# Performance work log

Hardware: AMD Instinct MI355X
Metric: run time of the kernel (lower is better)

The kernel has to match this reference:

```python
import jax, jax.numpy as jnp
import numpy as np

EPS = 1e-06

def rotate_half(x):
    d = x.shape[-1] // 2
    return jnp.concatenate([-x[..., d:], x[..., :d]], axis=-1)

def rmsnorm(x, w):
    rms = jnp.sqrt(jnp.mean(x * x, axis=-1, keepdims=True) + EPS)
    return (x / rms) * w

def setup_inputs() -> dict:
    key = jax.random.key(0)
    ks = jax.random.split(key, 12)
    H, Hq, Hkv, Dh, S, C = 2048, 16, 8, 128, 1, 16384
    sc = 0.02
    return {
        "hidden_states": jax.random.normal(ks[0], (1, 1, S, H), jnp.float32),
        "cos": jax.random.uniform(ks[1], (1, 1, S, Dh), jnp.float32),
        "sin": jax.random.uniform(ks[2], (1, 1, S, Dh), jnp.float32),
        "attention_mask": jnp.zeros((1, 1, S, C + S), jnp.float32),
        "k_cache": jax.random.normal(ks[3], (Hkv, Dh, C), jnp.float32),
        "v_cache": jax.random.normal(ks[4], (Hkv, C, Dh), jnp.float32),
        "Wq": jax.random.normal(ks[5], (Hq, Dh, H), jnp.float32) * sc,
        "Wk": jax.random.normal(ks[6], (Hkv, Dh, H), jnp.float32) * sc,
        "Wv": jax.random.normal(ks[7], (Hkv, Dh, H), jnp.float32) * sc,
        "Wo": jax.random.normal(ks[8], (H, Hq * Dh), jnp.float32) * sc,
        "q_norm_w": jnp.ones((Dh,), jnp.float32),
        "k_norm_w": jnp.ones((Dh,), jnp.float32),
    }

def reference(hidden_states, cos, sin, attention_mask, k_cache, v_cache, Wq, Wk, Wv, Wo, q_norm_w, k_norm_w):
    S = hidden_states.shape[2]
    Hq, Dh = Wq.shape[0], Wq.shape[1]
    Hkv = Wk.shape[0]
    g = Hq // Hkv
    x = hidden_states.reshape(S, -1)                      # [S, H]
    # per-head 1x1 conv == per-head linear; batched as einsum
    q = rmsnorm(jnp.einsum('sh,qdh->qsd', x, Wq), q_norm_w)   # [Hq, S, Dh]
    k = rmsnorm(jnp.einsum('sh,kdh->ksd', x, Wk), k_norm_w)   # [Hkv, S, Dh]
    v = jnp.einsum('sh,kdh->ksd', x, Wv)                      # [Hkv, S, Dh]
    c = cos.reshape(S, Dh)
    s = sin.reshape(S, Dh)
    q = q * c + rotate_half(q) * s
    k_new = k * c + rotate_half(k) * s
    # KV cache concat: k stored transposed [Hkv, Dh, C]
    k_full = jnp.concatenate([k_cache, jnp.swapaxes(k_new, 1, 2)], axis=2)  # [Hkv, Dh, C+S]
    v_full = jnp.concatenate([v_cache, v], axis=1)                          # [Hkv, C+S, Dh]
    kf = jnp.repeat(k_full, g, axis=0)                    # GQA expand -> [Hq, Dh, C+S]
    vf = jnp.repeat(v_full, g, axis=0)                    # [Hq, C+S, Dh]
    scaling = Dh ** -0.5
    scores = jnp.einsum('qsd,qdc->qsc', q, kf) * scaling + attention_mask.reshape(1, S, -1)
    probs = jax.nn.softmax(scores, axis=-1)
    out = jnp.einsum('qsc,qcd->qsd', probs, vf)           # [Hq, S, Dh]
    out = jnp.transpose(out, (1, 0, 2)).reshape(S, Hq * Dh)  # head-major last dim
    attn = out @ Wo.T                                     # o_proj 1x1 conv
    return attn.reshape(1, 1, S, -1), k_new, v
```

## Files before the change

### kernel.cpp

```cpp
#include <hip/hip_runtime.h>
#include <math.h>
#include <stddef.h>

#define HQ   16
#define HKV  8
#define DH   128
#define HID  2048
#define CC   16384
#define NCH  64
#define CHUNK 256


__global__ void k_qkv(const float* __restrict__ x,
                      const float* __restrict__ Wq,
                      const float* __restrict__ Wk,
                      const float* __restrict__ Wv,
                      float* __restrict__ raw){
  int wave = threadIdx.x >> 6, lane = threadIdx.x & 63;
  int e = blockIdx.x * 4 + wave;
  const float* W;
  if (e < 2048)      W = Wq + (size_t)e * HID;
  else if (e < 3072) W = Wk + (size_t)(e - 2048) * HID;
  else               W = Wv + (size_t)(e - 3072) * HID;
  float acc = 0.f;
  #pragma unroll
  for (int j = 0; j < 4; ++j){
    int base = (j * 64 + lane) * 8;
    float4 a0 = *(const float4*)(x + base);
    float4 a1 = *(const float4*)(x + base + 4);
    float4 b0 = *(const float4*)(W + base);
    float4 b1 = *(const float4*)(W + base + 4);
    acc += a0.x*b0.x + a0.y*b0.y + a0.z*b0.z + a0.w*b0.w
         + a1.x*b1.x + a1.y*b1.y + a1.z*b1.z + a1.w*b1.w;
  }
  #pragma unroll
  for (int off = 32; off; off >>= 1) acc += __shfl_down(acc, off, 64);
  if (lane == 0) raw[e] = acc;
}

__global__ void k_normrope(const float* __restrict__ raw,
                           const float* __restrict__ cosb,
                           const float* __restrict__ sinb,
                           const float* __restrict__ qw,
                           const float* __restrict__ kw,
                           float* __restrict__ qf,
                           float* __restrict__ kf,
                           float* __restrict__ out){
  __shared__ float lds[DH];
  __shared__ float wsum[2];
  int b = blockIdx.x, t = threadIdx.x;
  if (b >= 24){
    int h = b - 24;
    out[3072 + h * DH + t] = raw[3072 + h * DH + t];
    return;
  }
  bool isq = (b < 16);
  int h = isq ? b : b - 16;
  float val = isq ? raw[h * DH + t] : raw[2048 + h * DH + t];
  float ss = val * val;
  #pragma unroll
  for (int off = 32; off; off >>= 1) ss += __shfl_down(ss, off, 64);
  if ((t & 63) == 0) wsum[t >> 6] = ss;
  __syncthreads();
  float rms = sqrtf((wsum[0] + wsum[1]) / 128.f + 1e-6f);
  float w = isq ? qw[t] : kw[t];
  float normed = val / rms * w;
  lds[t] = normed;
  __syncthreads();
  float rot = (t < 64) ? -lds[t + 64] : lds[t - 64];
  float res = normed * cosb[t] + rot * sinb[t];
  if (isq) qf[h * DH + t] = res;
  else { kf[h * DH + t] = res; out[2048 + h * DH + t] = res; }
}

__global__ void k_flash(const float* __restrict__ qf,
                        const float* __restrict__ kcache,
                        const float* __restrict__ vcache,
                        const float* __restrict__ mask,
                        float* __restrict__ opart,
                        float2* __restrict__ ml){
  __shared__ float q_s[2][DH];
  __shared__ float sc_part[4][2][CHUNK];
  __shared__ float p_s[2][CHUNK];
  __shared__ float part[2][8][DH];
  __shared__ float red[8];
  int kv = blockIdx.x >> 6, ch = blockIdx.x & 63;
  int c0 = ch << 8;
  int t = threadIdx.x;
  q_s[t >> 7][t & 127] = qf[(kv * 2 + (t >> 7)) * DH + (t & 127)];
  __syncthreads();
  const float scale = 0.08838834764831845f;

  {
    int dg = t >> 6, ln = t & 63;
    const float* kp = kcache + (size_t)kv * DH * CC + (size_t)(dg * 32) * CC + (c0 + ln * 4);
    float a00 = 0.f, a01 = 0.f, a02 = 0.f, a03 = 0.f;
    float a10 = 0.f, a11 = 0.f, a12 = 0.f, a13 = 0.f;
    #pragma unroll 8
    for (int dd = 0; dd < 32; ++dd){
      float4 kk = *(const float4*)(kp + (size_t)dd * CC);
      float q0 = q_s[0][dg * 32 + dd], q1 = q_s[1][dg * 32 + dd];
      a00 += q0 * kk.x; a01 += q0 * kk.y; a02 += q0 * kk.z; a03 += q0 * kk.w;
      a10 += q1 * kk.x; a11 += q1 * kk.y; a12 += q1 * kk.z; a13 += q1 * kk.w;
    }
    *(float4*)&sc_part[dg][0][ln * 4] = make_float4(a00, a01, a02, a03);
    *(float4*)&sc_part[dg][1][ln * 4] = make_float4(a10, a11, a12, a13);
  }
  __syncthreads();

  float s0, s1;
  {
    float mk = mask[c0 + t];
    s0 = (sc_part[0][0][t] + sc_part[1][0][t] + sc_part[2][0][t] + sc_part[3][0][t]) * scale + mk;
    s1 = (sc_part[0][1][t] + sc_part[1][1][t] + sc_part[2][1][t] + sc_part[3][1][t]) * scale + mk;
  }
  int wv = t >> 6, ln = t & 63;
  float lmax0 = s0, lmax1 = s1;
  #pragma unroll
  for (int off = 32; off; off >>= 1){
    lmax0 = fmaxf(lmax0, __shfl_down(lmax0, off, 64));
    lmax1 = fmaxf(lmax1, __shfl_down(lmax1, off, 64));
  }
  if (ln == 0){ red[wv] = lmax0; red[4 + wv] = lmax1; }
  __syncthreads();
  float m0 = fmaxf(fmaxf(red[0], red[1]), fmaxf(red[2], red[3]));
  float m1 = fmaxf(fmaxf(red[4], red[5]), fmaxf(red[6], red[7]));
  float p0 = __expf(s0 - m0);
  float p1 = __expf(s1 - m1);
  p_s[0][t] = p0;
  p_s[1][t] = p1;
  float ls0 = p0, ls1 = p1;
  #pragma unroll
  for (int off = 32; off; off >>= 1){
    ls0 += __shfl_down(ls0, off, 64);
    ls1 += __shfl_down(ls1, off, 64);
  }
  __syncthreads();
  if (ln == 0){ red[wv] = ls0; red[4 + wv] = ls1; }
  __syncthreads();
  if (t == 0){
    float l0 = red[0] + red[1] + red[2] + red[3];
    float l1 = red[4] + red[5] + red[6] + red[7];
    ml[(size_t)(kv * 2)     * NCH + ch] = make_float2(m0, l0);
    ml[(size_t)(kv * 2 + 1) * NCH + ch] = make_float2(m1, l1);
  }

  {
    int s = t >> 5, d4 = (t & 31) * 4;
    const float* vbase = vcache + (size_t)kv * CC * DH + d4;
    float4 a0 = make_float4(0.f, 0.f, 0.f, 0.f);
    float4 a1 = make_float4(0.f, 0.f, 0.f, 0.f);
    #pragma unroll 4
    for (int i = 0; i < 32; ++i){
      int off = i * 8 + s;
      float pp0 = p_s[0][off];
      float pp1 = p_s[1][off];
      float4 v = *(const float4*)(vbase + (size_t)(c0 + off) * DH);
      a0.x += pp0 * v.x; a0.y += pp0 * v.y; a0.z += pp0 * v.z; a0.w += pp0 * v.w;
      a1.x += pp1 * v.x; a1.y += pp1 * v.y; a1.z += pp1 * v.z; a1.w += pp1 * v.w;
    }
    *(float4*)&part[0][s][d4] = a0;
    *(float4*)&part[1][s][d4] = a1;
  }
  __syncthreads();
  {
    int hh = t >> 7, d = t & 127;
    float o = 0.f;
    #pragma unroll
    for (int ss = 0; ss < 8; ++ss) o += part[hh][ss][d];
    int qh = kv * 2 + hh;
    opart[((size_t)qh * NCH + ch) * DH + d] = o;
  }
}

__global__ void k_combine(const float* __restrict__ opart,
                          const float2* __restrict__ ml,
                          const float* __restrict__ qf,
                          const float* __restrict__ kf,
                          const float* __restrict__ vnew,
                          const float* __restrict__ mask,
                          float* __restrict__ attn_in){
  __shared__ float red[2];
  int qh = blockIdx.x, d = threadIdx.x;
  int kv = qh >> 1;
  float M = -1e30f;
  #pragma unroll 8
  for (int ch = 0; ch < NCH; ++ch) M = fmaxf(M, ml[(size_t)qh * NCH + ch].x);
  float o = 0.f, L = 0.f;
  for (int ch = 0; ch < NCH; ++ch){
    float2 m = ml[(size_t)qh * NCH + ch];
    float w = __expf(m.x - M);
    L += m.y * w;
    o += w * opart[((size_t)qh * NCH + ch) * DH + d];
  }
  float prod = qf[qh * DH + d] * kf[kv * DH + d];
  float sum = prod;
  #pragma unroll
  for (int off = 32; off; off >>= 1) sum += __shfl_down(sum, off, 64);
  if ((d & 63) == 0) red[d >> 6] = sum;
  __syncthreads();
  float s_new = (red[0] + red[1]) * 0.08838834764831845f + mask[CC];
  float pn = __expf(s_new - M);
  L += pn;
  o += pn * vnew[kv * DH + d];
  attn_in[qh * DH + d] = o / L;
}

__global__ void k_oproj(const float* __restrict__ attn_in,
                        const float* __restrict__ Wo,
                        float* __restrict__ out){
  int wave = threadIdx.x >> 6, lane = threadIdx.x & 63;
  int e = blockIdx.x * 4 + wave;
  const float* W = Wo + (size_t)e * HID;
  float acc = 0.f;
  #pragma unroll
  for (int j = 0; j < 4; ++j){
    int base = (j * 64 + lane) * 8;
    float4 a0 = *(const float4*)(attn_in + base);
    float4 a1 = *(const float4*)(attn_in + base + 4);
    float4 b0 = *(const float4*)(W + base);
    float4 b1 = *(const float4*)(W + base + 4);
    acc += a0.x*b0.x + a0.y*b0.y + a0.z*b0.z + a0.w*b0.w
         + a1.x*b1.x + a1.y*b1.y + a1.z*b1.z + a1.w*b1.w;
  }
  #pragma unroll
  for (int off = 32; off; off >>= 1) acc += __shfl_down(acc, off, 64);
  if (lane == 0) out[e] = acc;
}

extern "C" void kernel_launch(void* const* d_in, const int* in_sizes, int n_in,
                              void* d_out, int out_size, void* d_ws, size_t ws_size,
                              hipStream_t stream){
  const float* x    = (const float*)d_in[0];
  const float* cosb = (const float*)d_in[1];
  const float* sinb = (const float*)d_in[2];
  const float* mask = (const float*)d_in[3];
  const float* kc   = (const float*)d_in[4];
  const float* vc   = (const float*)d_in[5];
  const float* Wq   = (const float*)d_in[6];
  const float* Wk   = (const float*)d_in[7];
  const float* Wv   = (const float*)d_in[8];
  const float* Wo   = (const float*)d_in[9];
  const float* qw   = (const float*)d_in[10];
  const float* kw   = (const float*)d_in[11];
  float* out = (float*)d_out;
  float* ws = (float*)d_ws;
  float* raw     = ws;
  float* qf      = ws + 4096;
  float* kf      = ws + 6144;
  float* opart   = ws + 8192;
  float2* ML     = (float2*)(ws + 139264);
  float* attn_in = ws + 141312;

  k_qkv     <<<1024, 256, 0, stream>>>(x, Wq, Wk, Wv, raw);
  k_normrope<<<32,   128, 0, stream>>>(raw, cosb, sinb, qw, kw, qf, kf, out);
  k_flash   <<<HKV * NCH, 256, 0, stream>>>(qf, kc, vc, mask, opart, ML);
  k_combine <<<HQ, 128, 0, stream>>>(opart, ML, qf, kf, raw + 3072, mask, attn_in);
  k_oproj   <<<512, 256, 0, stream>>>(attn_in, Wo, out);
}
```

Measured before the change: 216.4 us.

## Halve flash-decode chunk size, parallelize combine, and fuse V-copy into QKV

Splits the KV cache into 128 chunks of 128 positions instead of 64 chunks of 256, which doubles the number of attention blocks (1024) so more of the GPU's compute units are busy streaming K/V. The scoring phase now uses 8 depth groups of 16 per thread, and each head's softmax is reduced within its own half of the block. The combine kernel uses 512 threads, with four groups each merging 32 chunk partials plus a parallel max reduction, to absorb the doubled partial count. The V-output copy is folded into the QKV kernel so the norm/rope launch shrinks to 24 blocks. The cost is twice the partial-output traffic and more combine work.

```diff
diff --git a/kernel.cpp b/kernel.cpp
--- a/kernel.cpp
+++ b/kernel.cpp
@@ -7,15 +7,16 @@
 #define DH   128
 #define HID  2048
 #define CC   16384
-#define NCH  64
-#define CHUNK 256
+#define NCH  128
+#define CHUNK 128
 
 
 __global__ void k_qkv(const float* __restrict__ x,
                       const float* __restrict__ Wq,
                       const float* __restrict__ Wk,
                       const float* __restrict__ Wv,
-                      float* __restrict__ raw){
+                      float* __restrict__ raw,
+                      float* __restrict__ out){
   int wave = threadIdx.x >> 6, lane = threadIdx.x & 63;
   int e = blockIdx.x * 4 + wave;
   const float* W;
@@ -35,7 +36,10 @@
   }
   #pragma unroll
   for (int off = 32; off; off >>= 1) acc += __shfl_down(acc, off, 64);
-  if (lane == 0) raw[e] = acc;
+  if (lane == 0){
+    raw[e] = acc;
+    if (e >= 3072) out[e] = acc;
+  }
 }
 
 __global__ void k_normrope(const float* __restrict__ raw,
@@ -49,11 +53,6 @@
   __shared__ float lds[DH];
   __shared__ float wsum[2];
   int b = blockIdx.x, t = threadIdx.x;
-  if (b >= 24){
-    int h = b - 24;
-    out[3072 + h * DH + t] = raw[3072 + h * DH + t];
-    return;
-  }
   bool isq = (b < 16);
   int h = isq ? b : b - 16;
   float val = isq ? raw[h * DH + t] : raw[2048 + h * DH + t];
@@ -80,26 +79,26 @@
                         float* __restrict__ opart,
                         float2* __restrict__ ml){
   __shared__ float q_s[2][DH];
-  __shared__ float sc_part[4][2][CHUNK];
+  __shared__ float sc_part[8][2][CHUNK];
   __shared__ float p_s[2][CHUNK];
   __shared__ float part[2][8][DH];
   __shared__ float red[8];
-  int kv = blockIdx.x >> 6, ch = blockIdx.x & 63;
-  int c0 = ch << 8;
+  int kv = blockIdx.x >> 7, ch = blockIdx.x & 127;
+  int c0 = ch << 7;
   int t = threadIdx.x;
   q_s[t >> 7][t & 127] = qf[(kv * 2 + (t >> 7)) * DH + (t & 127)];
   __syncthreads();
   const float scale = 0.08838834764831845f;
 
   {
-    int dg = t >> 6, ln = t & 63;
-    const float* kp = kcache + (size_t)kv * DH * CC + (size_t)(dg * 32) * CC + (c0 + ln * 4);
+    int dg = t >> 5, ln = t & 31;
+    const float* kp = kcache + (size_t)kv * DH * CC + (size_t)(dg * 16) * CC + (c0 + ln * 4);
     float a00 = 0.f, a01 = 0.f, a02 = 0.f, a03 = 0.f;
     float a10 = 0.f, a11 = 0.f, a12 = 0.f, a13 = 0.f;
     #pragma unroll 8
-    for (int dd = 0; dd < 32; ++dd){
+    for (int dd = 0; dd < 16; ++dd){
       float4 kk = *(const float4*)(kp + (size_t)dd * CC);
-      float q0 = q_s[0][dg * 32 + dd], q1 = q_s[1][dg * 32 + dd];
+      float q0 = q_s[0][dg * 16 + dd], q1 = q_s[1][dg * 16 + dd];
       a00 += q0 * kk.x; a01 += q0 * kk.y; a02 += q0 * kk.z; a03 += q0 * kk.w;
       a10 += q1 * kk.x; a11 += q1 * kk.y; a12 += q1 * kk.z; a13 += q1 * kk.w;
     }
@@ -108,59 +107,49 @@
   }
   __syncthreads();
 
-  float s0, s1;
-  {
-    float mk = mask[c0 + t];
-    s0 = (sc_part[0][0][t] + sc_part[1][0][t] + sc_part[2][0][t] + sc_part[3][0][t]) * scale + mk;
-    s1 = (sc_part[0][1][t] + sc_part[1][1][t] + sc_part[2][1][t] + sc_part[3][1][t]) * scale + mk;
-  }
-  int wv = t >> 6, ln = t & 63;
-  float lmax0 = s0, lmax1 = s1;
-  #pragma unroll
-  for (int off = 32; off; off >>= 1){
-    lmax0 = fmaxf(lmax0, __shfl_down(lmax0, off, 64));
-    lmax1 = fmaxf(lmax1, __shfl_down(lmax1, off, 64));
-  }
-  if (ln == 0){ red[wv] = lmax0; red[4 + wv] = lmax1; }
-  __syncthreads();
-  float m0 = fmaxf(fmaxf(red[0], red[1]), fmaxf(red[2], red[3]));
-  float m1 = fmaxf(fmaxf(red[4], red[5]), fmaxf(red[6], red[7]));
-  float p0 = __expf(s0 - m0);
-  float p1 = __expf(s1 - m1);
-  p_s[0][t] = p0;
-  p_s[1][t] = p1;
-  float ls0 = p0, ls1 = p1;
-  #pragma unroll
-  for (int off = 32; off; off >>= 1){
-    ls0 += __shfl_down(ls0, off, 64);
-    ls1 += __shfl_down(ls1, off, 64);
-  }
-  __syncthreads();
-  if (ln == 0){ red[wv] = ls0; red[4 + wv] = ls1; }
-  __syncthreads();
-  if (t == 0){
-    float l0 = red[0] + red[1] + red[2] + red[3];
-    float l1 = red[4] + red[5] + red[6] + red[7];
-    ml[(size_t)(kv * 2)     * NCH + ch] = make_float2(m0, l0);
-    ml[(size_t)(kv * 2 + 1) * NCH + ch] = make_float2(m1, l1);
-  }
-
-  {
-    int s = t >> 5, d4 = (t & 31) * 4;
-    const float* vbase = vcache + (size_t)kv * CC * DH + d4;
+  int h = t >> 7, pos = t & 127;
+  float s;
+  {
+    float acc = 0.f;
+    #pragma unroll
+    for (int dg = 0; dg < 8; ++dg) acc += sc_part[dg][h][pos];
+    s = acc * scale + mask[c0 + pos];
+  }
+  int wv = t >> 6;
+  float lm = s;
+  #pragma unroll
+  for (int off = 32; off; off >>= 1) lm = fmaxf(lm, __shfl_down(lm, off, 64));
+  if ((t & 63) == 0) red[wv] = lm;
+  __syncthreads();
+  float m = fmaxf(red[h * 2], red[h * 2 + 1]);
+  float p = __expf(s - m);
+  p_s[h][pos] = p;
+  float lsum = p;
+  #pragma unroll
+  for (int off = 32; off; off >>= 1) lsum += __shfl_down(lsum, off, 64);
+  if ((t & 63) == 0) red[4 + wv] = lsum;
+  __syncthreads();
+  if ((t & 127) == 0){
+    float l = red[4 + h * 2] + red[5 + h * 2];
+    ml[(size_t)(kv * 2 + h) * NCH + ch] = make_float2(m, l);
+  }
+
+  {
+    int sl = t >> 5, d4 = (t & 31) * 4;
+    const float* vbase = vcache + (size_t)kv * CC * DH + (size_t)c0 * DH + d4;
     float4 a0 = make_float4(0.f, 0.f, 0.f, 0.f);
     float4 a1 = make_float4(0.f, 0.f, 0.f, 0.f);
-    #pragma unroll 4
-    for (int i = 0; i < 32; ++i){
-      int off = i * 8 + s;
+    #pragma unroll 8
+    for (int i = 0; i < 16; ++i){
+      int off = i * 8 + sl;
       float pp0 = p_s[0][off];
       float pp1 = p_s[1][off];
-      float4 v = *(const float4*)(vbase + (size_t)(c0 + off) * DH);
+      float4 v = *(const float4*)(vbase + (size_t)off * DH);
       a0.x += pp0 * v.x; a0.y += pp0 * v.y; a0.z += pp0 * v.z; a0.w += pp0 * v.w;
       a1.x += pp1 * v.x; a1.y += pp1 * v.y; a1.z += pp1 * v.z; a1.w += pp1 * v.w;
     }
-    *(float4*)&part[0][s][d4] = a0;
-    *(float4*)&part[1][s][d4] = a1;
+    *(float4*)&part[0][sl][d4] = a0;
+    *(float4*)&part[1][sl][d4] = a1;
   }
   __syncthreads();
   {
@@ -180,30 +169,46 @@
                           const float* __restrict__ vnew,
                           const float* __restrict__ mask,
                           float* __restrict__ attn_in){
-  __shared__ float red[2];
-  int qh = blockIdx.x, d = threadIdx.x;
+  __shared__ float osum[4][DH];
+  __shared__ float Ls[4];
+  __shared__ float redm[8];
+  __shared__ float redq[2];
+  int qh = blockIdx.x, t = threadIdx.x;
+  int g = t >> 7, d = t & 127;
   int kv = qh >> 1;
-  float M = -1e30f;
-  #pragma unroll 8
-  for (int ch = 0; ch < NCH; ++ch) M = fmaxf(M, ml[(size_t)qh * NCH + ch].x);
+  const float2* mlrow = ml + (size_t)qh * NCH;
+  float mm = mlrow[t & 127].x;
+  #pragma unroll
+  for (int off = 32; off; off >>= 1) mm = fmaxf(mm, __shfl_down(mm, off, 64));
+  if ((t & 63) == 0) redm[t >> 6] = mm;
+  __syncthreads();
+  float M = fmaxf(redm[0], redm[1]);
   float o = 0.f, L = 0.f;
-  for (int ch = 0; ch < NCH; ++ch){
-    float2 m = ml[(size_t)qh * NCH + ch];
-    float w = __expf(m.x - M);
-    L += m.y * w;
-    o += w * opart[((size_t)qh * NCH + ch) * DH + d];
-  }
-  float prod = qf[qh * DH + d] * kf[kv * DH + d];
-  float sum = prod;
-  #pragma unroll
-  for (int off = 32; off; off >>= 1) sum += __shfl_down(sum, off, 64);
-  if ((d & 63) == 0) red[d >> 6] = sum;
-  __syncthreads();
-  float s_new = (red[0] + red[1]) * 0.08838834764831845f + mask[CC];
-  float pn = __expf(s_new - M);
-  L += pn;
-  o += pn * vnew[kv * DH + d];
-  attn_in[qh * DH + d] = o / L;
+  int ch0 = g * 32;
+  #pragma unroll 4
+  for (int i = 0; i < 32; ++i){
+    float2 m2 = mlrow[ch0 + i];
+    float w = __expf(m2.x - M);
+    L += m2.y * w;
+    o += w * opart[((size_t)qh * NCH + ch0 + i) * DH + d];
+  }
+  osum[g][d] = o;
+  if (d == 0) Ls[g] = L;
+  if (t < DH){
+    float sum = qf[qh * DH + t] * kf[kv * DH + t];
+    #pragma unroll
+    for (int off = 32; off; off >>= 1) sum += __shfl_down(sum, off, 64);
+    if ((t & 63) == 0) redq[t >> 6] = sum;
+  }
+  __syncthreads();
+  if (t < DH){
+    float s_new = (redq[0] + redq[1]) * 0.08838834764831845f + mask[CC];
+    float pn = __expf(s_new - M);
+    float Lf = Ls[0] + Ls[1] + Ls[2] + Ls[3] + pn;
+    float of = osum[0][t] + osum[1][t] + osum[2][t] + osum[3][t]
+             + pn * vnew[kv * DH + t];
+    attn_in[qh * DH + t] = of / Lf;
+  }
 }
 
 __global__ void k_oproj(const float* __restrict__ attn_in,
@@ -249,12 +254,12 @@
   float* qf      = ws + 4096;
   float* kf      = ws + 6144;
   float* opart   = ws + 8192;
-  float2* ML     = (float2*)(ws + 139264);
-  float* attn_in = ws + 141312;
-
-  k_qkv     <<<1024, 256, 0, stream>>>(x, Wq, Wk, Wv, raw);
-  k_normrope<<<32,   128, 0, stream>>>(raw, cosb, sinb, qw, kw, qf, kf, out);
+  float2* ML     = (float2*)(ws + 270336);
+  float* attn_in = ws + 274432;
+
+  k_qkv     <<<1024, 256, 0, stream>>>(x, Wq, Wk, Wv, raw, out);
+  k_normrope<<<24,   128, 0, stream>>>(raw, cosb, sinb, qw, kw, qf, kf, out);
   k_flash   <<<HKV * NCH, 256, 0, stream>>>(qf, kc, vc, mask, opart, ML);
-  k_combine <<<HQ, 128, 0, stream>>>(opart, ML, qf, kf, raw + 3072, mask, attn_in);
+  k_combine <<<HQ, 512, 0, stream>>>(opart, ML, qf, kf, raw + 3072, mask, attn_in);
   k_oproj   <<<512, 256, 0, stream>>>(attn_in, Wo, out);
 }
```

Result: no change. 215.2 us (-0.6%).

## Fuse QKV with norm/rope and fuse attention, combine and o_proj via grid barrier

Applied to the files above, without the earlier changes.

Merges the QKV projection with RMSNorm and RoPE into one kernel that uses one 1024-thread block per head, with x staged in LDS. Flash attention, the cross-chunk combine and o_proj become a single kernel. A last-block-per-KV-head atomic counter does the combine, then a spin-wait grid barrier on a global counter gates the o_proj. This drops three launches and the global round trips between them. The QKV stage now streams its weights through only 32 blocks, which may limit bandwidth. The spin barrier relies on all 512 blocks being co-resident.

```diff
diff --git a/kernel.cpp b/kernel.cpp
--- a/kernel.cpp
+++ b/kernel.cpp
@@ -11,79 +11,108 @@
 #define CHUNK 256
 
 
-__global__ void k_qkv(const float* __restrict__ x,
-                      const float* __restrict__ Wq,
-                      const float* __restrict__ Wk,
-                      const float* __restrict__ Wv,
-                      float* __restrict__ raw){
-  int wave = threadIdx.x >> 6, lane = threadIdx.x & 63;
-  int e = blockIdx.x * 4 + wave;
-  const float* W;
-  if (e < 2048)      W = Wq + (size_t)e * HID;
-  else if (e < 3072) W = Wk + (size_t)(e - 2048) * HID;
-  else               W = Wv + (size_t)(e - 3072) * HID;
-  float acc = 0.f;
-  #pragma unroll
-  for (int j = 0; j < 4; ++j){
-    int base = (j * 64 + lane) * 8;
-    float4 a0 = *(const float4*)(x + base);
-    float4 a1 = *(const float4*)(x + base + 4);
-    float4 b0 = *(const float4*)(W + base);
-    float4 b1 = *(const float4*)(W + base + 4);
-    acc += a0.x*b0.x + a0.y*b0.y + a0.z*b0.z + a0.w*b0.w
-         + a1.x*b1.x + a1.y*b1.y + a1.z*b1.z + a1.w*b1.w;
-  }
-  #pragma unroll
-  for (int off = 32; off; off >>= 1) acc += __shfl_down(acc, off, 64);
-  if (lane == 0) raw[e] = acc;
+__global__ __launch_bounds__(1024) void k_qkvnorm(
+    const float* __restrict__ x,
+    const float* __restrict__ Wq,
+    const float* __restrict__ Wk,
+    const float* __restrict__ Wv,
+    const float* __restrict__ cosb,
+    const float* __restrict__ sinb,
+    const float* __restrict__ qw,
+    const float* __restrict__ kw,
+    float* __restrict__ qf,
+    float* __restrict__ kf,
+    float* __restrict__ vnew,
+    float* __restrict__ out,
+    int* __restrict__ ctr){
+  __shared__ float xs[HID];
+  __shared__ float rowval[DH];
+  __shared__ float wsum[2];
+  __shared__ float normed[DH];
+  int b = blockIdx.x, t = threadIdx.x;
+  if (b == 0 && t < 16) ctr[t] = 0;
+  xs[t] = x[t];
+  xs[t + 1024] = x[t + 1024];
+  __syncthreads();
+
+  bool isq = (b < 16), isk = (b >= 16 && b < 24);
+  int h = isq ? b : (isk ? b - 16 : b - 24);
+  const float* W = isq ? Wq : (isk ? Wk : Wv);
+  W += (size_t)h * DH * HID;
+
+  int w = t >> 6, l = t & 63;
+  float vals[8];
+  #pragma unroll
+  for (int oo = 0; oo < 8; ++oo){
+    const float* Wr = W + (size_t)(w * 8 + oo) * HID;
+    float acc = 0.f;
+    #pragma unroll
+    for (int j = 0; j < 8; ++j){
+      int idx = (j * 64 + l) * 4;
+      float4 wf = *(const float4*)(Wr + idx);
+      float4 xf = *(const float4*)(xs + idx);
+      acc += wf.x*xf.x + wf.y*xf.y + wf.z*xf.z + wf.w*xf.w;
+    }
+    vals[oo] = acc;
+  }
+  #pragma unroll
+  for (int oo = 0; oo < 8; ++oo){
+    float acc = vals[oo];
+    #pragma unroll
+    for (int off = 32; off; off >>= 1) acc += __shfl_down(acc, off, 64);
+    if (l == 0) rowval[w * 8 + oo] = acc;
+  }
+  __syncthreads();
+
+  float val = (t < DH) ? rowval[t] : 0.f;
+  if (!isq && !isk){
+    if (t < DH){
+      out[3072 + h * DH + t] = val;
+      vnew[h * DH + t] = val;
+    }
+    return;
+  }
+  float ss = val * val;
+  if (t < DH){
+    #pragma unroll
+    for (int off = 32; off; off >>= 1) ss += __shfl_down(ss, off, 64);
+    if ((t & 63) == 0) wsum[t >> 6] = ss;
+  }
+  __syncthreads();
+  float rms = sqrtf((wsum[0] + wsum[1]) * (1.f / 128.f) + 1e-6f);
+  if (t < DH){
+    float wgt = isq ? qw[t] : kw[t];
+    normed[t] = val / rms * wgt;
+  }
+  __syncthreads();
+  if (t < DH){
+    float nv = normed[t];
+    float rot = (t < 64) ? -normed[t + 64] : normed[t - 64];
+    float res = nv * cosb[t] + rot * sinb[t];
+    if (isq) qf[h * DH + t] = res;
+    else { kf[h * DH + t] = res; out[2048 + h * DH + t] = res; }
+  }
 }
 
-__global__ void k_normrope(const float* __restrict__ raw,
-                           const float* __restrict__ cosb,
-                           const float* __restrict__ sinb,
-                           const float* __restrict__ qw,
-                           const float* __restrict__ kw,
-                           float* __restrict__ qf,
-                           float* __restrict__ kf,
-                           float* __restrict__ out){
-  __shared__ float lds[DH];
-  __shared__ float wsum[2];
-  int b = blockIdx.x, t = threadIdx.x;
-  if (b >= 24){
-    int h = b - 24;
-    out[3072 + h * DH + t] = raw[3072 + h * DH + t];
-    return;
-  }
-  bool isq = (b < 16);
-  int h = isq ? b : b - 16;
-  float val = isq ? raw[h * DH + t] : raw[2048 + h * DH + t];
-  float ss = val * val;
-  #pragma unroll
-  for (int off = 32; off; off >>= 1) ss += __shfl_down(ss, off, 64);
-  if ((t & 63) == 0) wsum[t >> 6] = ss;
-  __syncthreads();
-  float rms = sqrtf((wsum[0] + wsum[1]) / 128.f + 1e-6f);
-  float w = isq ? qw[t] : kw[t];
-  float normed = val / rms * w;
-  lds[t] = normed;
-  __syncthreads();
-  float rot = (t < 64) ? -lds[t + 64] : lds[t - 64];
-  float res = normed * cosb[t] + rot * sinb[t];
-  if (isq) qf[h * DH + t] = res;
-  else { kf[h * DH + t] = res; out[2048 + h * DH + t] = res; }
-}
-
-__global__ void k_flash(const float* __restrict__ qf,
-                        const float* __restrict__ kcache,
-                        const float* __restrict__ vcache,
-                        const float* __restrict__ mask,
-                        float* __restrict__ opart,
-                        float2* __restrict__ ml){
+__global__ __launch_bounds__(256, 2) void k_attn(
+    const float* __restrict__ qf,
+    const float* __restrict__ kf,
+    const float* __restrict__ vnew,
+    const float* __restrict__ kcache,
+    const float* __restrict__ vcache,
+    const float* __restrict__ mask,
+    const float* __restrict__ Wo,
+    float* __restrict__ opart,
+    float2* __restrict__ ml,
+    float* __restrict__ attn_in,
+    int* __restrict__ ctr,
+    float* __restrict__ out){
   __shared__ float q_s[2][DH];
   __shared__ float sc_part[4][2][CHUNK];
   __shared__ float p_s[2][CHUNK];
   __shared__ float part[2][8][DH];
   __shared__ float red[8];
+  __shared__ int lastFlag;
   int kv = blockIdx.x >> 6, ch = blockIdx.x & 63;
   int c0 = ch << 8;
   int t = threadIdx.x;
@@ -146,21 +175,21 @@
   }
 
   {
-    int s = t >> 5, d4 = (t & 31) * 4;
+    int sl = t >> 5, d4 = (t & 31) * 4;
     const float* vbase = vcache + (size_t)kv * CC * DH + d4;
     float4 a0 = make_float4(0.f, 0.f, 0.f, 0.f);
     float4 a1 = make_float4(0.f, 0.f, 0.f, 0.f);
     #pragma unroll 4
     for (int i = 0; i < 32; ++i){
-      int off = i * 8 + s;
+      int off = i * 8 + sl;
       float pp0 = p_s[0][off];
       float pp1 = p_s[1][off];
       float4 v = *(const float4*)(vbase + (size_t)(c0 + off) * DH);
       a0.x += pp0 * v.x; a0.y += pp0 * v.y; a0.z += pp0 * v.z; a0.w += pp0 * v.w;
       a1.x += pp1 * v.x; a1.y += pp1 * v.y; a1.z += pp1 * v.z; a1.w += pp1 * v.w;
     }
-    *(float4*)&part[0][s][d4] = a0;
-    *(float4*)&part[1][s][d4] = a1;
+    *(float4*)&part[0][sl][d4] = a0;
+    *(float4*)&part[1][sl][d4] = a1;
   }
   __syncthreads();
   {
@@ -171,61 +200,69 @@
     int qh = kv * 2 + hh;
     opart[((size_t)qh * NCH + ch) * DH + d] = o;
   }
-}
-
-__global__ void k_combine(const float* __restrict__ opart,
-                          const float2* __restrict__ ml,
-                          const float* __restrict__ qf,
-                          const float* __restrict__ kf,
-                          const float* __restrict__ vnew,
-                          const float* __restrict__ mask,
-                          float* __restrict__ attn_in){
-  __shared__ float red[2];
-  int qh = blockIdx.x, d = threadIdx.x;
-  int kv = qh >> 1;
-  float M = -1e30f;
-  #pragma unroll 8
-  for (int ch = 0; ch < NCH; ++ch) M = fmaxf(M, ml[(size_t)qh * NCH + ch].x);
-  float o = 0.f, L = 0.f;
-  for (int ch = 0; ch < NCH; ++ch){
-    float2 m = ml[(size_t)qh * NCH + ch];
-    float w = __expf(m.x - M);
-    L += m.y * w;
-    o += w * opart[((size_t)qh * NCH + ch) * DH + d];
-  }
-  float prod = qf[qh * DH + d] * kf[kv * DH + d];
-  float sum = prod;
-  #pragma unroll
-  for (int off = 32; off; off >>= 1) sum += __shfl_down(sum, off, 64);
-  if ((d & 63) == 0) red[d >> 6] = sum;
-  __syncthreads();
-  float s_new = (red[0] + red[1]) * 0.08838834764831845f + mask[CC];
-  float pn = __expf(s_new - M);
-  L += pn;
-  o += pn * vnew[kv * DH + d];
-  attn_in[qh * DH + d] = o / L;
-}
-
-__global__ void k_oproj(const float* __restrict__ attn_in,
-                        const float* __restrict__ Wo,
-                        float* __restrict__ out){
-  int wave = threadIdx.x >> 6, lane = threadIdx.x & 63;
-  int e = blockIdx.x * 4 + wave;
-  const float* W = Wo + (size_t)e * HID;
-  float acc = 0.f;
-  #pragma unroll
-  for (int j = 0; j < 4; ++j){
-    int base = (j * 64 + lane) * 8;
-    float4 a0 = *(const float4*)(attn_in + base);
-    float4 a1 = *(const float4*)(attn_in + base + 4);
-    float4 b0 = *(const float4*)(W + base);
-    float4 b1 = *(const float4*)(W + base + 4);
-    acc += a0.x*b0.x + a0.y*b0.y + a0.z*b0.z + a0.w*b0.w
-         + a1.x*b1.x + a1.y*b1.y + a1.z*b1.z + a1.w*b1.w;
-  }
-  #pragma unroll
-  for (int off = 32; off; off >>= 1) acc += __shfl_down(acc, off, 64);
-  if (lane == 0) out[e] = acc;
+
+  __threadfence();
+  __syncthreads();
+  if (t == 0) lastFlag = (atomicAdd(&ctr[kv], 1) == NCH - 1) ? 1 : 0;
+  __syncthreads();
+  if (lastFlag){
+    __threadfence();
+    int h = t >> 7, d = t & 127;
+    int qh = kv * 2 + h;
+    const float2* mlrow = ml + (size_t)qh * NCH;
+    float M = -1e30f;
+    #pragma unroll 8
+    for (int c = 0; c < NCH; ++c) M = fmaxf(M, mlrow[c].x);
+    float oacc = 0.f, L = 0.f;
+    #pragma unroll 4
+    for (int c = 0; c < NCH; ++c){
+      float2 m2 = mlrow[c];
+      float wgt = __expf(m2.x - M);
+      L += m2.y * wgt;
+      oacc += wgt * opart[((size_t)qh * NCH + c) * DH + d];
+    }
+    float prod = qf[qh * DH + d] * kf[kv * DH + d];
+    #pragma unroll
+    for (int off = 32; off; off >>= 1) prod += __shfl_down(prod, off, 64);
+    if ((t & 63) == 0) red[t >> 6] = prod;
+    __syncthreads();
+    float s_new = (red[h * 2] + red[h * 2 + 1]) * scale + mask[CC];
+    float pn = __expf(s_new - M);
+    L += pn;
+    oacc += pn * vnew[kv * DH + d];
+    attn_in[qh * DH + d] = oacc / L;
+    __threadfence();
+    __syncthreads();
+    if (t == 0) atomicAdd(&ctr[8], 1);
+  }
+
+  if (t == 0){
+    while (__hip_atomic_load(&ctr[8], __ATOMIC_ACQUIRE, __HIP_MEMORY_SCOPE_AGENT) < HKV){
+      __builtin_amdgcn_s_sleep(2);
+    }
+  }
+  __syncthreads();
+  __threadfence();
+
+  {
+    int wv2 = t >> 6, l2 = t & 63;
+    int e = blockIdx.x * 4 + wv2;
+    const float* Wr = Wo + (size_t)e * HID;
+    float acc = 0.f;
+    #pragma unroll
+    for (int j = 0; j < 4; ++j){
+      int base = (j * 64 + l2) * 8;
+      float4 a0 = *(const float4*)(attn_in + base);
+      float4 a1 = *(const float4*)(attn_in + base + 4);
+      float4 b0 = *(const float4*)(Wr + base);
+      float4 b1 = *(const float4*)(Wr + base + 4);
+      acc += a0.x*b0.x + a0.y*b0.y + a0.z*b0.z + a0.w*b0.w
+           + a1.x*b1.x + a1.y*b1.y + a1.z*b1.z + a1.w*b1.w;
+    }
+    #pragma unroll
+    for (int off = 32; off; off >>= 1) acc += __shfl_down(acc, off, 64);
+    if (l2 == 0) out[e] = acc;
+  }
 }
 
 extern "C" void kernel_launch(void* const* d_in, const int* in_sizes, int n_in,
@@ -245,16 +282,16 @@
   const float* kw   = (const float*)d_in[11];
   float* out = (float*)d_out;
   float* ws = (float*)d_ws;
-  float* raw     = ws;
-  float* qf      = ws + 4096;
-  float* kf      = ws + 6144;
-  float* opart   = ws + 8192;
-  float2* ML     = (float2*)(ws + 139264);
-  float* attn_in = ws + 141312;
-
-  k_qkv     <<<1024, 256, 0, stream>>>(x, Wq, Wk, Wv, raw);
-  k_normrope<<<32,   128, 0, stream>>>(raw, cosb, sinb, qw, kw, qf, kf, out);
-  k_flash   <<<HKV * NCH, 256, 0, stream>>>(qf, kc, vc, mask, opart, ML);
-  k_combine <<<HQ, 128, 0, stream>>>(opart, ML, qf, kf, raw + 3072, mask, attn_in);
-  k_oproj   <<<512, 256, 0, stream>>>(attn_in, Wo, out);
+  float* qf      = ws;
+  float* kf      = ws + 2048;
+  float* vnew    = ws + 3072;
+  float* attn_in = ws + 4096;
+  float* opart   = ws + 6144;
+  float2* ML     = (float2*)(ws + 137216);
+  int*   ctr     = (int*)(ws + 139264);
+
+  k_qkvnorm<<<32, 1024, 0, stream>>>(x, Wq, Wk, Wv, cosb, sinb, qw, kw,
+                                     qf, kf, vnew, out, ctr);
+  k_attn<<<HKV * NCH, 256, 0, stream>>>(qf, kf, vnew, kc, vc, mask, Wo,
+                                        opart, ML, attn_in, ctr, out);
 }
```

Result: slower. 490.2 us (+126.5%).
